# Performance work log

Measured on AMD Instinct MI355X. Metric: run time of the kernel, lower is better.

The kernel has to match this reference:

```python
import jax, jax.numpy as jnp
import numpy as np

B, N, D = 4, 1024, 1024
T_ITER = 4
E_TYPES = 4  # edge_type_num; module loops over E_TYPES+1 with bitmask
ALPHA = 0.2


def _lin_w(key, out_f, in_f):
    # fan-avg uniform init from custom Linear
    bound = float(np.sqrt(3.0 / ((in_f + out_f) / 2.0)))
    return jax.random.uniform(key, (out_f, in_f), minval=-bound, maxval=bound, dtype=jnp.float32)


def setup_inputs() -> dict:
    key = jax.random.key(0)
    ks = jax.random.split(key, 32)
    inp = {}
    inp['ents'] = jax.random.normal(ks[0], (B, N, D), jnp.float32)
    inp['ent_mask'] = jnp.ones((B, N), jnp.float32)
    inp['q_encoding'] = jax.random.normal(ks[1], (B, D), jnp.float32)
    inp['adj'] = jax.random.randint(ks[2], (B, N, N), 0, E_TYPES + 1, dtype=jnp.int32)
    inp['types'] = 30  # bits 1..4 set -> edge types 1..4 active
    inp['init_mem'] = jax.random.normal(ks[3], (1, D), jnp.float32)
    inp['w_qin'] = _lin_w(ks[4], D, D); inp['b_qin'] = jnp.zeros((D,), jnp.float32)
    inp['w_qt'] = jnp.stack([_lin_w(ks[5 + t], D, D) for t in range(T_ITER)])
    inp['b_qt'] = jnp.zeros((T_ITER, D), jnp.float32)
    inp['w_pl'] = _lin_w(ks[9], D, D);  inp['b_pl'] = jnp.zeros((D,), jnp.float32)
    inp['w_pc'] = _lin_w(ks[10], D, D); inp['b_pc'] = jnp.zeros((D,), jnp.float32)
    inp['w_q'] = _lin_w(ks[11], D, 3 * D); inp['b_q'] = jnp.zeros((D,), jnp.float32)
    inp['w_k'] = _lin_w(ks[12], D, 3 * D); inp['b_k'] = jnp.zeros((D,), jnp.float32)
    inp['w_v'] = _lin_w(ks[13], D, 3 * D); inp['b_v'] = jnp.zeros((D,), jnp.float32)
    inp['w_pk'] = _lin_w(ks[14], D, D); inp['b_pk'] = jnp.zeros((D,), jnp.float32)
    inp['w_pv'] = _lin_w(ks[15], D, D); inp['b_pv'] = jnp.zeros((D,), jnp.float32)
    # wes: xavier_uniform(gain=1.414) on shape (2D, 1); stored flat as (E_TYPES, 2D)
    wb = 1.414 * float(np.sqrt(6.0 / (2 * D + 1)))
    inp['wes'] = jax.random.uniform(ks[16], (E_TYPES, 2 * D), minval=-wb, maxval=wb, dtype=jnp.float32)
    inp['w_mu'] = _lin_w(ks[17], D, 2 * D); inp['b_mu'] = jnp.zeros((D,), jnp.float32)
    inp['w_cb'] = _lin_w(ks[18], D, 2 * D); inp['b_cb'] = jnp.zeros((D,), jnp.float32)
    return inp


def _lin(x, w, b):
    return x @ w.T + b


def _qdgat_forward(ents, ent_mask, q_encoding, adj, types, init_mem,
                   w_qin, b_qin, w_qt, b_qt, w_pl, b_pl, w_pc, b_pc,
                   w_q, b_q, w_k, b_k, w_v, b_v, w_pk, b_pk, w_pv, b_pv,
                   wes, w_mu, b_mu, w_cb, b_cb):
    d = ents.shape[-1]
    x_loc = ents
    x_ctx = jnp.broadcast_to(init_mem, ents.shape)
    # eval mode: var-drop mask is ones scaled by ent_mask
    var_drop = ent_mask[:, :, None]
    adj_pos = adj > 0
    q_base = jax.nn.elu(_lin(q_encoding, w_qin, b_qin))
    n_types = wes.shape[0] + 1  # self.edge_type_num = edge_type_num + 1
    for t in range(T_ITER):
        cmd = _lin(q_base, w_qt[t], b_qt[t])                      # [B,D]
        xc = x_ctx * var_drop
        pl = _lin(x_loc, w_pl, b_pl)
        pc = _lin(xc, w_pc, b_pc)
        x_joint = jnp.concatenate([x_loc, xc, pl * pc], axis=-1)   # [B,N,3D]
        q = _lin(x_joint, w_q, b_q)                               # [B,N,D]
        k = _lin(x_joint, w_k, b_k) * _lin(cmd, w_pk, b_pk)[:, None, :]
        v = _lin(x_joint, w_v, b_v) * _lin(cmd, w_pv, b_pv)[:, None, :]
        # edge_score[b,i,j] = sum over active types T of (adj==T) * (q_i . we[:D] + k_j . we[D:])
        # equivalent to matmul((cat(q_i,k_j) * (adj==T)), we) without materializing [B,N,N,2D]
        edge_score = jnp.zeros(adj.shape, jnp.float32)
        for i in range(n_types):
            if (types >> i) & 1 == 1:
                w1, w2 = wes[i - 1, :d], wes[i - 1, d:]  # i=0 aliases wes[-1], as in torch
                s = (q @ w1)[:, :, None] + (k @ w2)[:, None, :]    # [B,N,N]
                edge_score = edge_score + jnp.where(adj == i, s, 0.0)
        e = jnp.where(edge_score > 0, edge_score, ALPHA * edge_score)  # leaky relu
        logits = jnp.where(adj_pos, e, jnp.float32(-9e15))
        prob = jax.nn.softmax(logits, axis=-1)                     # [B,N,N]
        message = jnp.einsum('bij,bjd->bid', prob, v)
        x_ctx = _lin(jnp.concatenate([xc, message], axis=-1), w_mu, b_mu)
    return _lin(jnp.concatenate([x_loc, x_ctx], axis=-1), w_cb, b_cb)


def reference(ents, ent_mask, q_encoding, adj, types, init_mem,
              w_qin, b_qin, w_qt, b_qt, w_pl, b_pl, w_pc, b_pc,
              w_q, b_q, w_k, b_k, w_v, b_v, w_pk, b_pk, w_pv, b_pv,
              wes, w_mu, b_mu, w_cb, b_cb):
    return _qdgat_forward(ents, ent_mask, q_encoding, adj, types, init_mem,
                          w_qin, b_qin, w_qt, b_qt, w_pl, b_pl, w_pc, b_pc,
                          w_q, b_q, w_k, b_k, w_v, b_v, w_pk, b_pk, w_pv, b_pv,
                          wes, w_mu, b_mu, w_cb, b_cb)
```

## Files before the change

### kernel.cpp

```cpp
#include <hip/hip_runtime.h>
#include <hip/hip_bf16.h>
#include <stdint.h>
#include <stddef.h>


typedef __hip_bfloat16 bf16;
typedef __attribute__((ext_vector_type(8))) short short8;
typedef __attribute__((ext_vector_type(4))) float floatx4;

#define NB 4
#define NN 1024
#define DD 1024
#define NT_ITER 4
#define MM (NB * NN)

static __device__ __forceinline__ float b2f(bf16 x) { return __bfloat162float(x); }
static __device__ __forceinline__ bf16 f2b(float x) { return __float2bfloat16(x); }
static __device__ __forceinline__ unsigned short f2bu(float x) {
    bf16 h = __float2bfloat16(x);
    unsigned short u;
    __builtin_memcpy(&u, &h, 2);
    return u;
}
static __device__ __forceinline__ float bu2f(unsigned short u) {
    unsigned int t = (unsigned int)u << 16;
    float f;
    __builtin_memcpy(&f, &t, 4);
    return f;
}

static __device__ __forceinline__ void gl_lds16(const void* g, void* l) {
    __builtin_amdgcn_global_load_lds(
        (const __attribute__((address_space(1))) unsigned int*)g,
        (__attribute__((address_space(3))) unsigned int*)l, 16, 0, 0);
}

__global__ void k_f2b(const float* __restrict__ src, bf16* __restrict__ dst, int n4) {
    int i = blockIdx.x * 256 + threadIdx.x;
    if (i >= n4) return;
    float4 v = ((const float4*)src)[i];
    ushort4 o;
    o.x = f2bu(v.x); o.y = f2bu(v.y); o.z = f2bu(v.z); o.w = f2bu(v.w);
    ((ushort4*)dst)[i] = o;
}

__global__ void k_transw(const float* __restrict__ src, bf16* __restrict__ dst) {
    __shared__ float tile[32][33];
    int c0 = blockIdx.x * 32;
    int r0 = blockIdx.y * 32;
    int tx = threadIdx.x, ty = threadIdx.y;
    for (int i = 0; i < 32; i += 8)
        tile[ty + i][tx] = src[(size_t)(r0 + ty + i) * 3072 + c0 + tx];
    __syncthreads();
    for (int i = 0; i < 32; i += 8)
        dst[(size_t)(c0 + ty + i) * 1024 + r0 + tx] = f2b(tile[tx][ty + i]);
}

__global__ void k_build_sc(const float* __restrict__ pk, const float* __restrict__ wes,
                           bf16* __restrict__ Aq, bf16* __restrict__ Ak) {
    int i = blockIdx.x * 256 + threadIdx.x;
    int half = i >> 16;
    int j = i & 65535;
    int row = j >> 10, d = j & 1023;
    if (half == 0) {
        Aq[j] = (row < 4) ? f2b(wes[(size_t)row * 2048 + d]) : f2b(0.f);
    } else {
        int t = row >> 4, b = (row >> 2) & 3, e = row & 3;
        Ak[j] = f2b(pk[((size_t)t * NB + b) * DD + d] * wes[(size_t)e * 2048 + 1024 + d]);
    }
}

__global__ __launch_bounds__(256) void k_qbase(const float* __restrict__ qenc, const float* __restrict__ w,
                                               const float* __restrict__ b, float* __restrict__ out) {
    int o = blockIdx.x * 4 + (threadIdx.x >> 6);
    int lane = threadIdx.x & 63;
    int n = o >> 2, r = o & 3;
    const float* xr = qenc + (size_t)r * DD;
    const float* wr = w + (size_t)n * DD;
    float s = 0.f;
    for (int d = lane; d < DD; d += 64) s += xr[d] * wr[d];
    for (int off = 32; off; off >>= 1) s += __shfl_down(s, off);
    if (lane == 0) {
        s += b[n];
        out[(size_t)r * DD + n] = s > 0.f ? s : (expf(s) - 1.0f);
    }
}

__global__ __launch_bounds__(256) void k_cmd(const float* __restrict__ qb, const float* __restrict__ w_qt,
                                             const float* __restrict__ b_qt, float* __restrict__ cmd) {
    int o = blockIdx.x * 4 + (threadIdx.x >> 6);
    int lane = threadIdx.x & 63;
    int r = o & 3, n = (o >> 2) & 1023, t = o >> 12;
    const float* xr = qb + (size_t)r * DD;
    const float* wr = w_qt + ((size_t)t * DD + n) * DD;
    float s = 0.f;
    for (int d = lane; d < DD; d += 64) s += xr[d] * wr[d];
    for (int off = 32; off; off >>= 1) s += __shfl_down(s, off);
    if (lane == 0) cmd[((size_t)t * NB + r) * DD + n] = s + b_qt[t * DD + n];
}

__global__ __launch_bounds__(256) void k_pkpv(const float* __restrict__ cmd,
                                              const float* __restrict__ w_pk, const float* __restrict__ b_pk,
                                              const float* __restrict__ w_pv, const float* __restrict__ b_pv,
                                              float* __restrict__ pk, float* __restrict__ pv) {
    int o = blockIdx.x * 4 + (threadIdx.x >> 6);
    int lane = threadIdx.x & 63;
    int n = o >> 5, half = (o >> 4) & 1, pair = o & 15;
    const float* xr = cmd + (size_t)pair * DD;
    const float* wr = (half ? w_pv : w_pk) + (size_t)n * DD;
    float s = 0.f;
    for (int d = lane; d < DD; d += 64) s += xr[d] * wr[d];
    for (int off = 32; off; off >>= 1) s += __shfl_down(s, off);
    if (lane == 0)
        (half ? pv : pk)[(size_t)pair * DD + n] = s + (half ? b_pv : b_pk)[n];
}

__global__ void k_consts(const float* __restrict__ b_q, const float* __restrict__ b_k,
                         const float* __restrict__ pk, const float* __restrict__ wes,
                         float* __restrict__ cq, float* __restrict__ ck) {
    int o = blockIdx.x;
    int lane = threadIdx.x;
    float s = 0.f;
    if (o < 4) {
        for (int d = lane; d < 1024; d += 64) s += b_q[d] * wes[(size_t)o * 2048 + d];
    } else {
        int oo = o - 4;
        int t = oo >> 4, b = (oo >> 2) & 3, e = oo & 3;
        for (int d = lane; d < 1024; d += 64)
            s += b_k[d] * pk[((size_t)t * NB + b) * DD + d] * wes[(size_t)e * 2048 + 1024 + d];
    }
    for (int off = 32; off; off >>= 1) s += __shfl_down(s, off);
    if (lane == 0) {
        if (o < 4) cq[o] = s;
        else ck[o - 4] = s;
    }
}

__global__ __launch_bounds__(256) void k_qakb2(const bf16* __restrict__ ents, const bf16* __restrict__ xc,
                                               const bf16* __restrict__ plpc,
                                               const float* __restrict__ wqtw, const float* __restrict__ wkeff_t,
                                               const float* __restrict__ cq, const float* __restrict__ ck_t,
                                               float* __restrict__ qa, float* __restrict__ kb) {
    __shared__ float red[4][8];
    int m = blockIdx.x;
    int b = m >> 10;
    int t = threadIdx.x;
    float aq[4] = {0.f, 0.f, 0.f, 0.f}, ak[4] = {0.f, 0.f, 0.f, 0.f};
    const bf16* rows[3] = {ents + (size_t)m * DD, xc + (size_t)m * DD, plpc + (size_t)m * DD};
#pragma unroll
    for (int c = 0; c < 3; ++c) {
        const bf16* row = rows[c];
        const float* wq = wqtw + c * 1024;
        const float* wk = wkeff_t + (size_t)b * 4 * 3072 + c * 1024;
        for (int d = t; d < 1024; d += 256) {
            float xv = b2f(row[d]);
#pragma unroll
            for (int e = 0; e < 4; ++e) {
                aq[e] += xv * wq[(size_t)e * 3072 + d];
                ak[e] += xv * wk[(size_t)e * 3072 + d];
            }
        }
    }
#pragma unroll
    for (int e = 0; e < 4; ++e) {
        float v = aq[e];
        for (int o = 32; o; o >>= 1) v += __shfl_down(v, o);
        if ((t & 63) == 0) red[t >> 6][e] = v;
        v = ak[e];
        for (int o = 32; o; o >>= 1) v += __shfl_down(v, o);
        if ((t & 63) == 0) red[t >> 6][e + 4] = v;
    }
    __syncthreads();
    if (t < 8) {
        float s = red[0][t] + red[1][t] + red[2][t] + red[3][t];
        if (t < 4) qa[(size_t)m * 4 + t] = s + cq[t];
        else kb[(size_t)m * 4 + (t - 4)] = s + ck_t[b * 4 + (t - 4)];
    }
}

__global__ void k_init(const bf16* __restrict__ initm_bf, const float* __restrict__ mask,
                       bf16* __restrict__ x_ctx, bf16* __restrict__ xc) {
    int i = blockIdx.x * 256 + threadIdx.x;
    uint4 v = ((const uint4*)initm_bf)[i & 127];
    ((uint4*)x_ctx)[i] = v;
    float mk = mask[i >> 7];
    unsigned short* u = (unsigned short*)&v;
#pragma unroll
    for (int j = 0; j < 8; ++j) u[j] = f2bu(bu2f(u[j]) * mk);
    ((uint4*)xc)[i] = v;
}

template <int WM>
__device__ __forceinline__ void gemm_core(
    const bf16* __restrict__ A0, const bf16* __restrict__ A1, const bf16* __restrict__ A2,
    const bf16* __restrict__ W, const float* __restrict__ bias, void* __restrict__ C,
    const void* __restrict__ mul, const float* __restrict__ addC, bf16* __restrict__ C2,
    int mulmode, int storef32, int nchunks, int ldw, int ldc,
    int bm, int bn) {
    constexpr int BM = WM * 2;
    constexpr int MI = WM / 16;
    constexpr int SEGS = (BM + 64) / 8;
    constexpr int SPW = SEGS / 4;
    __shared__ bf16 sAB[2][(BM + 64) * 64];

    const int t = threadIdx.x;
    const int lane = t & 63;
    const int w = t >> 6;
    const int wm = (w & 1) * WM, wn = (w >> 1) * 32;
    const int srow = lane >> 3;
    const int scol = ((lane & 7) * 8) ^ (srow << 3);

    floatx4 acc[MI][2];
#pragma unroll
    for (int i = 0; i < MI; ++i)
#pragma unroll
        for (int j = 0; j < 2; ++j) acc[i][j] = (floatx4){0.f, 0.f, 0.f, 0.f};

    const int lrow = lane & 15;
    const int kq = (lane >> 4) * 8;
    const int kx = (lane & 7) << 3;
    const int ktiles = nchunks * 16;

    auto stage = [&](int buf, int kt) {
        const int cidx = kt >> 4;
        const bf16* Ac = (cidx == 0) ? A0 : (cidx == 1 ? A1 : A2);
        const int klocal = (kt & 15) * 64;
        const int kglob = kt * 64;
#pragma unroll
        for (int s = 0; s < SPW; ++s) {
            int c = w * SPW + s;
            if (c < BM / 8) {
                const bf16* src = Ac + ((size_t)(bm * BM + c * 8 + srow)) * 1024 + klocal + scol;
                gl_lds16(src, &sAB[buf][c * 512]);
            } else {
                const bf16* src = W + ((size_t)(bn * 64 + (c - BM / 8) * 8 + srow)) * (size_t)ldw + kglob + scol;
                gl_lds16(src, &sAB[buf][c * 512]);
            }
        }
    };

    stage(0, 0);
    __syncthreads();
    int cur = 0;
    for (int kt = 0; kt < ktiles; ++kt) {
        if (kt + 1 < ktiles) stage(cur ^ 1, kt + 1);
#pragma unroll
        for (int ks = 0; ks < 2; ++ks) {
            const int ko = (ks * 32 + kq) ^ kx;
            short8 af[MI], bfr[2];
#pragma unroll
            for (int mi = 0; mi < MI; ++mi)
                af[mi] = *(const short8*)&sAB[cur][(wm + mi * 16 + lrow) * 64 + ko];
#pragma unroll
            for (int ni = 0; ni < 2; ++ni)
                bfr[ni] = *(const short8*)&sAB[cur][BM * 64 + (wn + ni * 16 + lrow) * 64 + ko];
#pragma unroll
            for (int mi = 0; mi < MI; ++mi)
#pragma unroll
                for (int ni = 0; ni < 2; ++ni)
                    acc[mi][ni] = __builtin_amdgcn_mfma_f32_16x16x32_bf16(af[mi], bfr[ni], acc[mi][ni], 0, 0, 0);
        }
        __syncthreads();
        cur ^= 1;
    }

    const int qrow = (lane >> 4) * 4;
#pragma unroll
    for (int mi = 0; mi < MI; ++mi) {
#pragma unroll
        for (int ni = 0; ni < 2; ++ni) {
            int gn = bn * 64 + wn + ni * 16 + lrow;
            float bv = bias ? bias[gn] : 0.f;
#pragma unroll
            for (int r = 0; r < 4; ++r) {
                int gm = bm * BM + wm + mi * 16 + qrow + r;
                size_t ci = (size_t)gm * (size_t)ldc + gn;
                float val = acc[mi][ni][r] + bv;
                if (addC) val += addC[ci];
                if (mulmode == 1)
                    val *= b2f(((const bf16*)mul)[(size_t)gm * 1024 + gn]);
                else if (mulmode == 2)
                    val *= ((const float*)mul)[(size_t)(gm >> 10) * 1024 + gn];
                if (storef32) {
                    ((float*)C)[ci] = val;
                } else {
                    ((bf16*)C)[ci] = f2b(val);
                    if (mulmode == 3)
                        C2[ci] = f2b(val * ((const float*)mul)[gm]);
                }
            }
        }
    }
}

template <int WM>
__global__ __launch_bounds__(256) void k_gemm_t(
    const bf16* __restrict__ A0, const bf16* __restrict__ A1, const bf16* __restrict__ A2,
    const bf16* __restrict__ W, const float* __restrict__ bias, void* __restrict__ C,
    const void* __restrict__ mul, const float* __restrict__ addC, bf16* __restrict__ C2,
    int mulmode, int storef32, int nchunks, int ldw, int ldc,
    long long sA, long long sW, long long sC) {
    int bz = blockIdx.z;
    const bf16* A0b = A0 + (size_t)bz * sA;
    const bf16* Wb = W + (size_t)bz * sW;
    void* Cb = storef32 ? (void*)((float*)C + (size_t)bz * sC)
                        : (void*)((bf16*)C + (size_t)bz * sC);
    gemm_core<WM>(A0b, A1, A2, Wb, bias, Cb, mul, addC, C2, mulmode, storef32, nchunks, ldw, ldc,
                  blockIdx.x, blockIdx.y);
}

__global__ void k_transpose(const bf16* __restrict__ v, bf16* __restrict__ vT) {
    __shared__ bf16 tile[32][33];
    int b = blockIdx.z;
    int n0 = blockIdx.x * 32, d0 = blockIdx.y * 32;
    int tx = threadIdx.x, ty = threadIdx.y;
    for (int i = 0; i < 32; i += 8)
        tile[ty + i][tx] = v[((size_t)b * NN + n0 + ty + i) * DD + d0 + tx];
    __syncthreads();
    for (int i = 0; i < 32; i += 8)
        vT[((size_t)b * DD + d0 + ty + i) * NN + n0 + tx] = tile[tx][ty + i];
}

__global__ __launch_bounds__(256) void k_attn(const int* __restrict__ adj, const float* __restrict__ qa,
                                              const float* __restrict__ kb, const int* __restrict__ typesPtr,
                                              bf16* __restrict__ prob) {
    __shared__ float lg[NN];
    __shared__ float red[4];
    __shared__ float red2[4];
    int m = blockIdx.x;
    int b = m >> 10;
    int t = threadIdx.x;
    int types = typesPtr[0];
    float qa4[4];
#pragma unroll
    for (int e = 0; e < 4; ++e) qa4[e] = qa[(size_t)m * 4 + e];
    const int* arow = adj + (size_t)m * NN;
    const float* kbb = kb + (size_t)(b << 10) * 4;

    float lmax = -3.0e38f;
    for (int j = t; j < NN; j += 256) {
        int a = arow[j];
        float l;
        if (a == 0) {
            l = -9.0e15f;
        } else if ((types >> a) & 1) {
            float s = qa4[a - 1] + kbb[(size_t)j * 4 + (a - 1)];
            l = s > 0.f ? s : 0.2f * s;
        } else {
            l = 0.f;
        }
        lg[j] = l;
        lmax = fmaxf(lmax, l);
    }
    for (int o = 32; o > 0; o >>= 1) lmax = fmaxf(lmax, __shfl_down(lmax, o));
    if ((t & 63) == 0) red[t >> 6] = lmax;
    __syncthreads();
    lmax = fmaxf(fmaxf(red[0], red[1]), fmaxf(red[2], red[3]));

    float lsum = 0.f;
    for (int j = t; j < NN; j += 256) {
        float ex = __expf(lg[j] - lmax);
        lg[j] = ex;
        lsum += ex;
    }
    for (int o = 32; o > 0; o >>= 1) lsum += __shfl_down(lsum, o);
    if ((t & 63) == 0) red2[t >> 6] = lsum;
    __syncthreads();
    lsum = red2[0] + red2[1] + red2[2] + red2[3];
    float inv = 1.0f / lsum;

    bf16* prow = prob + (size_t)m * NN;
    for (int j = t; j < NN; j += 256) prow[j] = f2b(lg[j] * inv);
}

extern "C" void kernel_launch(void* const* d_in, const int* in_sizes, int n_in,
                              void* d_out, int out_size, void* d_ws, size_t ws_size,
                              hipStream_t stream) {
    const float* ents = (const float*)d_in[0];
    const float* mask = (const float*)d_in[1];
    const float* qenc = (const float*)d_in[2];
    const int* adj = (const int*)d_in[3];
    const int* types = (const int*)d_in[4];
    const float* initm = (const float*)d_in[5];
    const float* w_qin = (const float*)d_in[6];
    const float* b_qin = (const float*)d_in[7];
    const float* w_qt = (const float*)d_in[8];
    const float* b_qt = (const float*)d_in[9];
    const float* w_pl = (const float*)d_in[10];
    const float* b_pl = (const float*)d_in[11];
    const float* w_pc = (const float*)d_in[12];
    const float* b_pc = (const float*)d_in[13];
    const float* w_q = (const float*)d_in[14];
    const float* b_q = (const float*)d_in[15];
    const float* w_k = (const float*)d_in[16];
    const float* b_k = (const float*)d_in[17];
    const float* w_v = (const float*)d_in[18];
    const float* b_v = (const float*)d_in[19];
    const float* w_pk = (const float*)d_in[20];
    const float* b_pk = (const float*)d_in[21];
    const float* w_pv = (const float*)d_in[22];
    const float* b_pv = (const float*)d_in[23];
    const float* wes = (const float*)d_in[24];
    const float* w_mu = (const float*)d_in[25];
    const float* b_mu = (const float*)d_in[26];
    const float* w_cb = (const float*)d_in[27];
    const float* b_cb = (const float*)d_in[28];
    (void)in_sizes; (void)n_in; (void)out_size; (void)ws_size;

    char* p = (char*)d_ws;
    auto carve = [&](size_t bytes) {
        char* r = p;
        p += (bytes + 255) & ~(size_t)255;
        return r;
    };
    float* q_base = (float*)carve((size_t)NB * DD * 4);
    float* cmd = (float*)carve((size_t)NT_ITER * NB * DD * 4);
    float* pk = (float*)carve((size_t)NT_ITER * NB * DD * 4);
    float* pv = (float*)carve((size_t)NT_ITER * NB * DD * 4);
    float* qa = (float*)carve((size_t)MM * 4 * 4);
    float* kb = (float*)carve((size_t)MM * 4 * 4);
    float* wqtw = (float*)carve((size_t)64 * 3072 * 4);
    float* wkeff = (float*)carve((size_t)64 * 3072 * 4);
    float* cq = (float*)carve(4 * 4);
    float* ck = (float*)carve(64 * 4);
    float* vent = (float*)carve((size_t)MM * DD * 4);
    bf16* initm_bf = (bf16*)carve((size_t)DD * 2);
    bf16* ents_bf = (bf16*)carve((size_t)MM * DD * 2);
    bf16* wpl_bf = (bf16*)carve((size_t)DD * DD * 2);
    bf16* wpc_bf = (bf16*)carve((size_t)DD * DD * 2);
    bf16* wv_bf = (bf16*)carve((size_t)DD * 3 * DD * 2);
    bf16* wmu_bf = (bf16*)carve((size_t)DD * 2 * DD * 2);
    bf16* wcb_bf = (bf16*)carve((size_t)DD * 2 * DD * 2);
    bf16* wqT_bf = (bf16*)carve((size_t)3 * DD * DD * 2);
    bf16* wkT_bf = (bf16*)carve((size_t)3 * DD * DD * 2);
    bf16* Aq = (bf16*)carve((size_t)64 * DD * 2);
    bf16* Ak = (bf16*)carve((size_t)64 * DD * 2);
    bf16* x_ctx = (bf16*)carve((size_t)MM * DD * 2);
    bf16* xc = (bf16*)carve((size_t)MM * DD * 2);
    bf16* pl = (bf16*)carve((size_t)MM * DD * 2);
    bf16* plpc = (bf16*)carve((size_t)MM * DD * 2);
    bf16* vbuf = (bf16*)carve((size_t)MM * DD * 2);
    bf16* msg = (bf16*)carve((size_t)MM * DD * 2);
    bf16* prob = (bf16*)carve((size_t)NB * NN * NN * 2);
    bf16* vT = plpc;

    const dim3 blk(256);
    const dim3 g128(32, 16, 1);
    const dim3 gMsg(8, 16, NB);
    const dim3 gPre(1, 48, 1);

    k_f2b<<<1, blk, 0, stream>>>(initm, initm_bf, DD / 4);
    k_f2b<<<4096, blk, 0, stream>>>(ents, ents_bf, MM * DD / 4);
    k_f2b<<<1024, blk, 0, stream>>>(w_pl, wpl_bf, DD * DD / 4);
    k_f2b<<<1024, blk, 0, stream>>>(w_pc, wpc_bf, DD * DD / 4);
    k_f2b<<<3072, blk, 0, stream>>>(w_v, wv_bf, DD * 3 * DD / 4);
    k_f2b<<<2048, blk, 0, stream>>>(w_mu, wmu_bf, DD * 2 * DD / 4);
    k_f2b<<<2048, blk, 0, stream>>>(w_cb, wcb_bf, DD * 2 * DD / 4);
    k_transw<<<dim3(96, 32), dim3(32, 8), 0, stream>>>(w_q, wqT_bf);
    k_transw<<<dim3(96, 32), dim3(32, 8), 0, stream>>>(w_k, wkT_bf);

    k_qbase<<<1024, blk, 0, stream>>>(qenc, w_qin, b_qin, q_base);
    k_cmd<<<4096, blk, 0, stream>>>(q_base, w_qt, b_qt, cmd);
    k_pkpv<<<8192, blk, 0, stream>>>(cmd, w_pk, b_pk, w_pv, b_pv, pk, pv);
    k_init<<<2048, blk, 0, stream>>>(initm_bf, mask, x_ctx, xc);

    k_build_sc<<<512, blk, 0, stream>>>(pk, wes, Aq, Ak);
    k_consts<<<68, 64, 0, stream>>>(b_q, b_k, pk, wes, cq, ck);
    k_gemm_t<32><<<gPre, blk, 0, stream>>>(Aq, nullptr, nullptr, wqT_bf, nullptr, wqtw,
                                           nullptr, nullptr, nullptr, 0, 1, 1, 1024, 3072, 0, 0, 0);
    k_gemm_t<32><<<gPre, blk, 0, stream>>>(Ak, nullptr, nullptr, wkT_bf, nullptr, wkeff,
                                           nullptr, nullptr, nullptr, 0, 1, 1, 1024, 3072, 0, 0, 0);

    k_gemm_t<64><<<g128, blk, 0, stream>>>(ents_bf, nullptr, nullptr, wpl_bf, b_pl, pl,
                                           nullptr, nullptr, nullptr, 0, 0, 1, 1024, 1024, 0, 0, 0);
    k_gemm_t<64><<<g128, blk, 0, stream>>>(ents_bf, nullptr, nullptr, wv_bf, nullptr, vent,
                                           nullptr, nullptr, nullptr, 0, 1, 1, 3072, 1024, 0, 0, 0);

    for (int t = 0; t < NT_ITER; ++t) {
        k_gemm_t<64><<<g128, blk, 0, stream>>>(xc, nullptr, nullptr, wpc_bf, b_pc, plpc,
                                               pl, nullptr, nullptr, 1, 0, 1, 1024, 1024, 0, 0, 0);
        k_gemm_t<64><<<g128, blk, 0, stream>>>(xc, plpc, nullptr, wv_bf + 1024, b_v, vbuf,
                                               pv + (size_t)t * NB * DD, vent, nullptr, 2, 0, 2, 3072, 1024, 0, 0, 0);
        k_qakb2<<<4096, blk, 0, stream>>>(ents_bf, xc, plpc,
                                          wqtw, wkeff + (size_t)t * 16 * 3072,
                                          cq, ck + t * 16, qa, kb);
        k_transpose<<<dim3(32, 32, NB), dim3(32, 8), 0, stream>>>(vbuf, vT);
        k_attn<<<4096, blk, 0, stream>>>(adj, qa, kb, types, prob);
        k_gemm_t<64><<<gMsg, blk, 0, stream>>>(prob, nullptr, nullptr, vT, nullptr, msg,
                                               nullptr, nullptr, nullptr, 0, 0, 1, 1024, 1024,
                                               (long long)NN * NN, (long long)DD * NN, (long long)NN * DD);
        k_gemm_t<64><<<g128, blk, 0, stream>>>(xc, msg, nullptr, wmu_bf, b_mu, x_ctx,
                                               mask, nullptr, xc, 3, 0, 2, 2048, 1024, 0, 0, 0);
    }
    k_gemm_t<64><<<g128, blk, 0, stream>>>(ents_bf, x_ctx, nullptr, wcb_bf, b_cb, (float*)d_out,
                                           nullptr, nullptr, nullptr, 0, 1, 2, 2048, 1024, 0, 0, 0);
}
```

Baseline: 966.9 us.

## Triple-buffer GEMM LDS staging with vmcnt waits and single barrier per k-tile

Changes the bf16 MFMA GEMM core from double to triple buffering of LDS tiles. Loads for tile k+2 are issued after the fragments for tile k are read into registers. Each k-step now uses one explicit vmcnt wait and one s_barrier in place of two __syncthreads. MFMA issue priority is raised with s_setprio. This aims to hide global-load latency and cut barrier stalls, at the cost of more LDS per block (possible occupancy loss) and more fragment registers.

```diff
diff --git a/kernel.cpp b/kernel.cpp
--- a/kernel.cpp
+++ b/kernel.cpp
@@ -33,6 +33,13 @@
     __builtin_amdgcn_global_load_lds(
         (const __attribute__((address_space(1))) unsigned int*)g,
         (__attribute__((address_space(3))) unsigned int*)l, 16, 0, 0);
+}
+
+template <int N>
+static __device__ __forceinline__ void s_wait_vmcnt() {
+    if constexpr (N == 0)      asm volatile("s_waitcnt vmcnt(0)" ::: "memory");
+    else if constexpr (N == 4) asm volatile("s_waitcnt vmcnt(4)" ::: "memory");
+    else if constexpr (N == 6) asm volatile("s_waitcnt vmcnt(6)" ::: "memory");
 }
 
 __global__ void k_f2b(const float* __restrict__ src, bf16* __restrict__ dst, int n4) {
@@ -201,7 +208,7 @@
     constexpr int MI = WM / 16;
     constexpr int SEGS = (BM + 64) / 8;
     constexpr int SPW = SEGS / 4;
-    __shared__ bf16 sAB[2][(BM + 64) * 64];
+    __shared__ bf16 sAB[3][(BM + 64) * 64];
 
     const int t = threadIdx.x;
     const int lane = t & 63;
@@ -240,28 +247,38 @@
     };
 
     stage(0, 0);
-    __syncthreads();
-    int cur = 0;
+    if (ktiles > 1) stage(1, 1);
+    int cur = 0, sb = 2;
     for (int kt = 0; kt < ktiles; ++kt) {
-        if (kt + 1 < ktiles) stage(cur ^ 1, kt + 1);
+        if (kt + 1 < ktiles) s_wait_vmcnt<SPW>();
+        else s_wait_vmcnt<0>();
+        __builtin_amdgcn_s_barrier();
+        __builtin_amdgcn_sched_barrier(0);
+        short8 af[2][MI], bfr[2][2];
 #pragma unroll
         for (int ks = 0; ks < 2; ++ks) {
             const int ko = (ks * 32 + kq) ^ kx;
-            short8 af[MI], bfr[2];
 #pragma unroll
             for (int mi = 0; mi < MI; ++mi)
-                af[mi] = *(const short8*)&sAB[cur][(wm + mi * 16 + lrow) * 64 + ko];
+                af[ks][mi] = *(const short8*)&sAB[cur][(wm + mi * 16 + lrow) * 64 + ko];
 #pragma unroll
             for (int ni = 0; ni < 2; ++ni)
-                bfr[ni] = *(const short8*)&sAB[cur][BM * 64 + (wn + ni * 16 + lrow) * 64 + ko];
+                bfr[ks][ni] = *(const short8*)&sAB[cur][BM * 64 + (wn + ni * 16 + lrow) * 64 + ko];
+        }
+        if (kt + 2 < ktiles) stage(sb, kt + 2);
+        __builtin_amdgcn_s_setprio(1);
+#pragma unroll
+        for (int ks = 0; ks < 2; ++ks)
 #pragma unroll
             for (int mi = 0; mi < MI; ++mi)
 #pragma unroll
                 for (int ni = 0; ni < 2; ++ni)
-                    acc[mi][ni] = __builtin_amdgcn_mfma_f32_16x16x32_bf16(af[mi], bfr[ni], acc[mi][ni], 0, 0, 0);
-        }
-        __syncthreads();
-        cur ^= 1;
+                    acc[mi][ni] = __builtin_amdgcn_mfma_f32_16x16x32_bf16(af[ks][mi], bfr[ks][ni], acc[mi][ni], 0, 0, 0);
+        __builtin_amdgcn_s_setprio(0);
+        asm volatile("s_waitcnt lgkmcnt(0)" ::: "memory");
+        __builtin_amdgcn_sched_barrier(0);
+        cur = (cur == 2) ? 0 : cur + 1;
+        sb = (sb == 2) ? 0 : sb + 1;
     }
 
     const int qrow = (lane >> 4) * 4;
```

After: 943.8 us. -2.4%, faster.
